# Kernel tuning notes

Hardware: AMD Instinct MI355X
Metric: run time of the kernel (lower is better)

The kernel has to match this reference:

```python
import jax, jax.numpy as jnp
import numpy as np

TEMP_MIN, TEMP_MAX = 0.1, 1.0
NEG = -1e30  # finite stand-in for -inf (grad-safe)


def _cumlse(x, axis, reverse=False):
    # cumulative logsumexp along `axis`
    return jax.lax.associative_scan(jnp.logaddexp, x, axis=axis, reverse=reverse)


def setup_inputs() -> dict:
    key = jax.random.key(0)
    k1, k2, k3 = jax.random.split(key, 3)
    B, T, M, C = 16, 512, 2048, 512
    return {
        "text_embeddings": jax.random.normal(k1, (B, T, C), jnp.float32),
        "mel_embeddings": jax.random.normal(k2, (B, M, C), jnp.float32),
        "noise_uniform": jax.random.uniform(k3, (B, T, M), jnp.float32, 1e-6, 1.0 - 1e-6),
        "temperature_ratio": jnp.full((1,), 0.5, jnp.float32),
    }


def reference(text_embeddings, mel_embeddings, noise_uniform, temperature_ratio):
    B, T, C = text_embeddings.shape
    M, Cm = mel_embeddings.shape[1], mel_embeddings.shape[2]
    energy = jnp.einsum('btc,bmc->btm', text_embeddings, mel_embeddings) / np.float32(np.sqrt(C * Cm))
    temperature = TEMP_MIN + (TEMP_MAX - TEMP_MIN) * jnp.reshape(temperature_ratio, ())
    gumbel = -jnp.log(-jnp.log(noise_uniform))
    # torch code computes e = exp((energy+noise)/T); we keep it in log domain:
    log_e = (energy + gumbel) / temperature                      # [B,T,M]
    # log_cond_prob[b,t,k,j] = log_e[b,t,k] - log_S[b,t,j] if k>=j else -inf
    # (the torch 4D triu-masked tensor, never materialized here)
    log_S = _cumlse(log_e, axis=2, reverse=True)                 # log sum_{k>=j} e[b,t,k]

    # alpha DP: alpha[b,i,k+1] = lse_{j<=k}(alpha[b,i-1,j] + lcp[b,i-1,k,j])
    #         = log_e[b,i-1,k] + lse_{j<=k}(alpha[b,i-1,j] - log_S[b,i-1,j])
    alpha0 = jnp.concatenate([jnp.zeros((B, 1), log_e.dtype),
                              jnp.full((B, M), NEG, log_e.dtype)], axis=1)  # [B,M+1]
    def alpha_step(prev, xs):
        le_t, ls_t = xs                                          # [B,M] each
        inner = _cumlse(prev[:, :M] - ls_t, axis=1)              # lse over j<=k
        new = jnp.concatenate([jnp.full((B, 1), NEG, le_t.dtype), le_t + inner], axis=1)
        return new, new
    _, alphas = jax.lax.scan(alpha_step, alpha0,
                             (jnp.swapaxes(log_e, 0, 1), jnp.swapaxes(log_S, 0, 1)))
    alpha_tail = jnp.swapaxes(alphas, 0, 1)[:, :, 1:]            # alpha[:,1:,1:] -> [B,T,M]

    # beta DP (intended backward recurrence; torch source had an undefined
    # `cond_prob` and a shape bug here):
    # beta[b,i,j] = lse_{k>=j}(beta[b,i+1,k] + log_e[b,i,k]) - log_S[b,i,j]
    beta_T = jnp.zeros((B, M), log_e.dtype).at[:, M - 1].set(1.0)  # faithful odd init =1
    def beta_step(nxt, xs):
        le_t, ls_t = xs
        new = _cumlse(nxt + le_t, axis=1, reverse=True) - ls_t
        return new, new
    _, betas = jax.lax.scan(beta_step, beta_T,
                            (jnp.swapaxes(log_e, 0, 1)[:T - 1], jnp.swapaxes(log_S, 0, 1)[:T - 1]),
                            reverse=True)
    beta = jnp.swapaxes(jnp.concatenate([betas, beta_T[None]], axis=0), 0, 1)  # [B,T,M]

    gamma = alpha_tail + beta
    gamma_log = gamma - jax.scipy.special.logsumexp(gamma, axis=1, keepdims=True)
    # torch uses raw (log-domain) gamma in the bmm; kept faithful
    expanded = jnp.einsum('btm,btc->bmc', gamma, text_embeddings)  # [B,M,C]
    return gamma_log, expanded
```

## Files before the change

### kernel.cpp

```cpp
#include <hip/hip_runtime.h>

#define B_  16
#define T_  512
#define M_  2048
#define C_  512
#define NEGV (-1e30f)
#define L2E 1.4426950408889634f
#define LN2 0.69314718055994531f

typedef unsigned short u16;
typedef unsigned int   u32;
using bf16x8 = __attribute__((ext_vector_type(8))) short;
using f32x4  = __attribute__((ext_vector_type(4))) float;

__device__ __forceinline__ u16 f2bf(float x) {
  u32 u = __float_as_uint(x);
  return (u16)((u + 0x7FFFu + ((u >> 16) & 1u)) >> 16);
}
__device__ __forceinline__ float bf2f(u16 u) {
  return __uint_as_float(((u32)u) << 16);
}
__device__ __forceinline__ float rdlane63(float x) {
  return __int_as_float(__builtin_amdgcn_readlane(__float_as_int(x), 63));
}

__device__ __forceinline__ float wscan_add(float x) {
  x += __int_as_float(__builtin_amdgcn_update_dpp(0, __float_as_int(x), 0x111, 0xF, 0xF, true));
  x += __int_as_float(__builtin_amdgcn_update_dpp(0, __float_as_int(x), 0x112, 0xF, 0xF, true));
  x += __int_as_float(__builtin_amdgcn_update_dpp(0, __float_as_int(x), 0x114, 0xF, 0xF, true));
  x += __int_as_float(__builtin_amdgcn_update_dpp(0, __float_as_int(x), 0x118, 0xF, 0xF, true));
  x += __int_as_float(__builtin_amdgcn_update_dpp(0, __float_as_int(x), 0x142, 0xA, 0xF, true));
  x += __int_as_float(__builtin_amdgcn_update_dpp(0, __float_as_int(x), 0x143, 0xC, 0xF, true));
  return x;
}
__device__ __forceinline__ float dpp_shr1(float x) {
  return __int_as_float(__builtin_amdgcn_update_dpp(0, __float_as_int(x), 0x138, 0xF, 0xF, true));
}

__launch_bounds__(256)
__global__ void k1_energy(const float* __restrict__ text, const float* __restrict__ mel,
                          const float* __restrict__ noise, const float* __restrict__ ratio,
                          u16* __restrict__ ttbuf)
{
  __shared__ __align__(16) short As[128][40];
  __shared__ __align__(16) short Bs[128][40];
  const int b   = blockIdx.z;
  const int t0  = blockIdx.x * 128;
  const int m0  = blockIdx.y * 128;
  const int tid = threadIdx.x;
  const int lane = tid & 63, wid = tid >> 6;
  const int wr = wid >> 1, wc = wid & 1;
  const float* Ab = text + (size_t)b * T_ * C_;
  const float* Bb = mel  + (size_t)b * M_ * C_;
  f32x4 acc[4][4];
#pragma unroll
  for (int i = 0; i < 4; ++i)
#pragma unroll
    for (int j = 0; j < 4; ++j) acc[i][j] = (f32x4){0.f, 0.f, 0.f, 0.f};

  const int kq = (tid & 7) * 4;
  const int rb = tid >> 3;
  for (int kk = 0; kk < C_; kk += 32) {
    __syncthreads();
#pragma unroll
    for (int it = 0; it < 4; ++it) {
      int r = rb + it * 32;
      float4 va = *(const float4*)(Ab + (size_t)(t0 + r) * C_ + kk + kq);
      As[r][kq + 0] = (short)f2bf(va.x); As[r][kq + 1] = (short)f2bf(va.y);
      As[r][kq + 2] = (short)f2bf(va.z); As[r][kq + 3] = (short)f2bf(va.w);
      float4 vb = *(const float4*)(Bb + (size_t)(m0 + r) * C_ + kk + kq);
      Bs[r][kq + 0] = (short)f2bf(vb.x); Bs[r][kq + 1] = (short)f2bf(vb.y);
      Bs[r][kq + 2] = (short)f2bf(vb.z); Bs[r][kq + 3] = (short)f2bf(vb.w);
    }
    __syncthreads();
    const int k0 = (lane >> 4) * 8;
    bf16x8 af[4], bfr[4];
#pragma unroll
    for (int i = 0; i < 4; ++i) {
      af[i]  = *(const bf16x8*)&As[wr * 64 + i * 16 + (lane & 15)][k0];
      bfr[i] = *(const bf16x8*)&Bs[wc * 64 + i * 16 + (lane & 15)][k0];
    }
#pragma unroll
    for (int i = 0; i < 4; ++i)
#pragma unroll
      for (int j = 0; j < 4; ++j)
        acc[i][j] = __builtin_amdgcn_mfma_f32_16x16x32_bf16(af[i], bfr[j], acc[i][j], 0, 0, 0);
  }
  const float invT = 1.0f / (0.1f + 0.9f * ratio[0]);
  const float D2 = 14.5f * invT * L2E;
#pragma unroll
  for (int i = 0; i < 4; ++i) {
#pragma unroll
    for (int j = 0; j < 4; ++j) {
#pragma unroll
      for (int rr = 0; rr < 4; ++rr) {
        int t = t0 + wr * 64 + i * 16 + (lane >> 4) * 4 + rr;
        int m = m0 + wc * 64 + j * 16 + (lane & 15);
        size_t idx = ((size_t)b * T_ + t) * M_ + m;
        float en = acc[i][j][rr] * (1.0f / 512.0f);
        float u  = noise[idx];
        float nl = -LN2 * __builtin_amdgcn_logf(u);
        float g  = -LN2 * __builtin_amdgcn_logf(nl);
        float le = (en + g) * invT;
        float tv = __builtin_amdgcn_exp2f(__builtin_fmaf(le, L2E, -D2));
        ttbuf[idx] = f2bf(tv);
      }
    }
  }
}

__launch_bounds__(256)
__global__ void k2r(const u16* __restrict__ ttbuf, u16* __restrict__ Rbuf)
{
  const size_t row = blockIdx.x;
  const u16* src = ttbuf + row * M_;
  u16* dst = Rbuf + row * M_;
  const int tid = threadIdx.x, lane = tid & 63, wid = tid >> 6;
  const int c0 = tid * 8;
  uint4 w = *(const uint4*)(src + c0);
  float x[8];
  x[0] = __uint_as_float(w.x << 16); x[1] = __uint_as_float(w.x & 0xFFFF0000u);
  x[2] = __uint_as_float(w.y << 16); x[3] = __uint_as_float(w.y & 0xFFFF0000u);
  x[4] = __uint_as_float(w.z << 16); x[5] = __uint_as_float(w.z & 0xFFFF0000u);
  x[6] = __uint_as_float(w.w << 16); x[7] = __uint_as_float(w.w & 0xFFFF0000u);
#pragma unroll
  for (int i = 6; i >= 0; --i) x[i] += x[i + 1];
  float v = x[0];
#pragma unroll
  for (int d = 1; d < 64; d <<= 1) {
    float t = __shfl_down(v, d);
    if (lane < 64 - d) v += t;
  }
  float e = __shfl_down(v, 1);
  if (lane == 63) e = 0.f;
  __shared__ float part[4];
  if (lane == 0) part[wid] = v;
  __syncthreads();
  float we = 0.f;
  for (int w2 = wid + 1; w2 < 4; ++w2) we += part[w2];
  float off = e + we;
  u32 o[4];
#pragma unroll
  for (int i = 0; i < 4; ++i) {
    float r0 = __builtin_amdgcn_rcpf(x[2*i]     + off);
    float r1 = __builtin_amdgcn_rcpf(x[2*i + 1] + off);
    o[i] = __builtin_amdgcn_perm(__float_as_uint(r1), __float_as_uint(r0), 0x07060302u);
  }
  *(uint4*)(dst + c0) = make_uint4(o[0], o[1], o[2], o[3]);
}

__launch_bounds__(512)
__global__ void k3a_partial(const float* __restrict__ text, float* __restrict__ partial)
{
  const int b = blockIdx.x >> 3, ch = blockIdx.x & 7, c = threadIdx.x;
  const float* tb = text + (size_t)b * T_ * C_ + (size_t)ch * 64 * C_ + c;
  float s = 0.f;
#pragma unroll 8
  for (int tt = 0; tt < 64; ++tt) s += tb[(size_t)tt * C_];
  partial[((size_t)b * 8 + ch) * C_ + c] = s;
}

__launch_bounds__(512)
__global__ void k3b_suffix(const float* __restrict__ text, const float* __restrict__ partial,
                           float* __restrict__ suffix)
{
  const int b = blockIdx.x >> 3, ch = blockIdx.x & 7, c = threadIdx.x;
  float off = 0.f;
  for (int ch2 = ch + 1; ch2 < 8; ++ch2) off += partial[((size_t)b * 8 + ch2) * C_ + c];
  const float* tb = text + (size_t)b * T_ * C_ + (size_t)ch * 64 * C_ + c;
  float* sb = suffix + (size_t)b * (T_ + 1) * C_ + (size_t)ch * 64 * C_ + c;
  if (ch == 7) sb[(size_t)64 * C_] = 0.f;
  float s = off;
  for (int tt = 63; tt >= 0; --tt) {
    s += tb[(size_t)tt * C_];
    sb[(size_t)tt * C_] = s;
  }
}

__launch_bounds__(256)
__global__ void k3t_textT(const float* __restrict__ text, u16* __restrict__ textT)
{
  __shared__ u16 tile[64][66];
  const int b  = blockIdx.z;
  const int t0 = blockIdx.x * 64;
  const int c0 = blockIdx.y * 64;
  const int tid = threadIdx.x;
  const int j = tid & 63, i4 = tid >> 6;
#pragma unroll
  for (int it = 0; it < 16; ++it) {
    int i = it * 4 + i4;
    tile[i][j] = f2bf(text[((size_t)b * T_ + t0 + i) * C_ + c0 + j]);
  }
  __syncthreads();
#pragma unroll
  for (int it = 0; it < 16; ++it) {
    int cc = it * 4 + i4;
    textT[((size_t)b * C_ + c0 + cc) * T_ + t0 + j] = tile[j][cc];
  }
}

__launch_bounds__(64, 1)
__global__ void k4_dp(const u16* __restrict__ ttbuf, const u16* __restrict__ Rbuf,
                      u16* __restrict__ Abuf, u16* __restrict__ Bbuf,
                      float* __restrict__ CAa, float* __restrict__ CBa)
{
  const int blk = blockIdx.x;
  const int b   = blk & 15;
  const int lane = threadIdx.x & 63;
  const u16* TT = ttbuf + (size_t)b * T_ * M_;
  const u16* RR = Rbuf  + (size_t)b * T_ * M_;
  uint4 rawT[2][4], rawR[2][4];
  float arr[32], cum[32], A[32];
  float Cv = 0.f;

  if (blk < 16) {
    const int c0 = lane * 32;
    u16* AO = Abuf + (size_t)b * T_ * M_;
    float* CO = CAa + (size_t)b * T_;

#define TLDA(BUF, R) { \
    const uint4* pt_ = (const uint4*)(TT + (size_t)(R) * M_ + c0); \
    const uint4* pr_ = (const uint4*)(RR + (size_t)(R) * M_ + c0); \
    rawT[BUF][0]=pt_[0]; rawT[BUF][1]=pt_[1]; rawT[BUF][2]=pt_[2]; rawT[BUF][3]=pt_[3]; \
    rawR[BUF][0]=pr_[0]; rawR[BUF][1]=pr_[1]; rawR[BUF][2]=pr_[2]; rawR[BUF][3]=pr_[3]; }

#define FOLD2A(E, W) { \
    cum[E]   = A[(E)-1] * __uint_as_float((W) << 16); \
    cum[(E)+1] = A[E]   * __uint_as_float((W) & 0xFFFF0000u); }

#define ASTEP(BUF, RIDX, FIRST) { \
    const int r_ = (RIDX); \
     \
    _Pragma("unroll") for (int q = 0; q < 4; ++q) { \
      u32 w0 = rawT[BUF][q].x, w1 = rawT[BUF][q].y, w2 = rawT[BUF][q].z, w3 = rawT[BUF][q].w; \
      arr[8*q+0] = __uint_as_float(w0 << 16); arr[8*q+1] = __uint_as_float(w0 & 0xFFFF0000u); \
      arr[8*q+2] = __uint_as_float(w1 << 16); arr[8*q+3] = __uint_as_float(w1 & 0xFFFF0000u); \
      arr[8*q+4] = __uint_as_float(w2 << 16); arr[8*q+5] = __uint_as_float(w2 & 0xFFFF0000u); \
      arr[8*q+6] = __uint_as_float(w3 << 16); arr[8*q+7] = __uint_as_float(w3 & 0xFFFF0000u); } \
     \
    { float am1 = dpp_shr1(A[31]); \
      if (FIRST) am1 = (lane == 0) ? 1.f : am1; \
      u32 v0 = rawR[BUF][0].x; \
      cum[0] = am1 * __uint_as_float(v0 << 16); \
      cum[1] = A[0] * __uint_as_float(v0 & 0xFFFF0000u); } \
    FOLD2A(2, rawR[BUF][0].y) FOLD2A(4, rawR[BUF][0].z) FOLD2A(6, rawR[BUF][0].w) \
    _Pragma("unroll") for (int q = 1; q < 4; ++q) { \
      FOLD2A(8*q+0, rawR[BUF][q].x) FOLD2A(8*q+2, rawR[BUF][q].y) \
      FOLD2A(8*q+4, rawR[BUF][q].z) FOLD2A(8*q+6, rawR[BUF][q].w) } \
     \
    TLDA(BUF, (r_ + 2 < T_) ? r_ + 2 : T_ - 1) \
    __builtin_amdgcn_sched_barrier(0); \
     \
    _Pragma("unroll") for (int c = 0; c < 4; ++c) \
      _Pragma("unroll") for (int k = 1; k < 8; ++k) cum[8*c+k] += cum[8*c+k-1]; \
    { float Te = (cum[7] + cum[15]) + (cum[23] + cum[31]); \
      float v_ = wscan_add(Te); \
      float exw = v_ - Te; \
      float Zt = rdlane63(v_); \
      float f0 = exw, f1 = f0+cum[7], f2 = f1+cum[15], f3 = f2+cum[23]; \
      float Zc = fmaxf(Zt, 1e-35f); \
      float zr = __builtin_amdgcn_rcpf(Zc); \
      Cv += LN2 * __builtin_amdgcn_logf(Zc); \
      if (lane == 0) CO[r_] = Cv; \
      float fz0 = f0*zr, fz1 = f1*zr, fz2 = f2*zr, fz3 = f3*zr; \
      _Pragma("unroll") for (int k = 0; k < 8; ++k) { \
        A[k]    = arr[k]    * __builtin_fmaf(cum[k],    zr, fz0); \
        A[8+k]  = arr[8+k]  * __builtin_fmaf(cum[8+k],  zr, fz1); \
        A[16+k] = arr[16+k] * __builtin_fmaf(cum[16+k], zr, fz2); \
        A[24+k] = arr[24+k] * __builtin_fmaf(cum[24+k], zr, fz3); } } \
    { u32 w_[16]; \
      _Pragma("unroll") for (int d = 0; d < 16; ++d) \
        w_[d] = __builtin_amdgcn_perm(__float_as_uint(A[2*d+1]), __float_as_uint(A[2*d]), 0x07060302u); \
      uint4* op = (uint4*)(AO + (size_t)r_ * M_ + c0); \
      op[0] = make_uint4(w_[0],w_[1],w_[2],w_[3]); \
      op[1] = make_uint4(w_[4],w_[5],w_[6],w_[7]); \
      op[2] = make_uint4(w_[8],w_[9],w_[10],w_[11]); \
      op[3] = make_uint4(w_[12],w_[13],w_[14],w_[15]); } \
  }

#pragma unroll
    for (int e = 0; e < 32; ++e) A[e] = 0.f;
    TLDA(0, 0) TLDA(1, 1)
    ASTEP(0, 0, true)
    ASTEP(1, 1, false)
    for (int r = 2; r < T_; r += 2) {
      ASTEP(0, r, false)
      ASTEP(1, r + 1, false)
    }
  } else {
    const int jb = M_ - 32 - lane * 32;
    u16* BO = Bbuf + (size_t)b * T_ * M_;
    float* CO = CBa + (size_t)b * T_;

#define TLDB(BUF, R) { \
    const uint4* pt_ = (const uint4*)(TT + (size_t)(R) * M_ + jb); \
    const uint4* pr_ = (const uint4*)(RR + (size_t)(R) * M_ + jb); \
    rawT[BUF][0]=pt_[0]; rawT[BUF][1]=pt_[1]; rawT[BUF][2]=pt_[2]; rawT[BUF][3]=pt_[3]; \
    rawR[BUF][0]=pr_[0]; rawR[BUF][1]=pr_[1]; rawR[BUF][2]=pr_[2]; rawR[BUF][3]=pr_[3]; }

#define FOLD2B(E, W) { \
    cum[E]     = A[E]     * __uint_as_float((W) << 16); \
    cum[(E)-1] = A[(E)-1] * __uint_as_float((W) & 0xFFFF0000u); }

#define BSTEP(BUF, TIDX) { \
    const int t_ = (TIDX); \
     \
    _Pragma("unroll") for (int q = 0; q < 4; ++q) { \
      u32 w0 = rawR[BUF][q].x, w1 = rawR[BUF][q].y, w2 = rawR[BUF][q].z, w3 = rawR[BUF][q].w; \
      arr[31-8*q] = __uint_as_float(w0 << 16); arr[30-8*q] = __uint_as_float(w0 & 0xFFFF0000u); \
      arr[29-8*q] = __uint_as_float(w1 << 16); arr[28-8*q] = __uint_as_float(w1 & 0xFFFF0000u); \
      arr[27-8*q] = __uint_as_float(w2 << 16); arr[26-8*q] = __uint_as_float(w2 & 0xFFFF0000u); \
      arr[25-8*q] = __uint_as_float(w3 << 16); arr[24-8*q] = __uint_as_float(w3 & 0xFFFF0000u); } \
     \
    _Pragma("unroll") for (int q = 0; q < 4; ++q) { \
      FOLD2B(31-8*q, rawT[BUF][q].x) FOLD2B(29-8*q, rawT[BUF][q].y) \
      FOLD2B(27-8*q, rawT[BUF][q].z) FOLD2B(25-8*q, rawT[BUF][q].w) } \
    { int tp_ = t_ - 2; if (tp_ < 0) tp_ = 0; TLDB(BUF, tp_) } \
    __builtin_amdgcn_sched_barrier(0); \
     \
    _Pragma("unroll") for (int c = 0; c < 4; ++c) \
      _Pragma("unroll") for (int k = 1; k < 8; ++k) cum[8*c+k] += cum[8*c+k-1]; \
    { float Te = (cum[7] + cum[15]) + (cum[23] + cum[31]); \
      float v_ = wscan_add(Te); \
      float exw = v_ - Te; \
      float Zb = rdlane63(v_); \
      float f0 = exw, f1 = f0+cum[7], f2 = f1+cum[15], f3 = f2+cum[23]; \
      float Zc = fmaxf(Zb, 1e-35f); \
      float zr = __builtin_amdgcn_rcpf(Zc); \
      Cv += LN2 * __builtin_amdgcn_logf(Zc); \
      float fz0 = f0*zr, fz1 = f1*zr, fz2 = f2*zr, fz3 = f3*zr; \
      _Pragma("unroll") for (int k = 0; k < 8; ++k) { \
        A[k]    = arr[k]    * __builtin_fmaf(cum[k],    zr, fz0); \
        A[8+k]  = arr[8+k]  * __builtin_fmaf(cum[8+k],  zr, fz1); \
        A[16+k] = arr[16+k] * __builtin_fmaf(cum[16+k], zr, fz2); \
        A[24+k] = arr[24+k] * __builtin_fmaf(cum[24+k], zr, fz3); } } \
    if (t_ >= 0) { \
      if (lane == 0) CO[t_] = Cv; \
      u32 w_[16]; \
      _Pragma("unroll") for (int d = 0; d < 16; ++d) \
        w_[d] = __builtin_amdgcn_perm(__float_as_uint(A[30-2*d]), __float_as_uint(A[31-2*d]), 0x07060302u); \
      uint4* op = (uint4*)(BO + (size_t)t_ * M_ + jb); \
      op[0] = make_uint4(w_[0],w_[1],w_[2],w_[3]); \
      op[1] = make_uint4(w_[4],w_[5],w_[6],w_[7]); \
      op[2] = make_uint4(w_[8],w_[9],w_[10],w_[11]); \
      op[3] = make_uint4(w_[12],w_[13],w_[14],w_[15]); } \
  }

#pragma unroll
    for (int e = 0; e < 32; ++e) A[e] = 1.f;
    if (lane == 0) A[0] = 2.718281828f;
    { u32 w_[16];
#pragma unroll
      for (int d = 0; d < 16; ++d)
        w_[d] = __builtin_amdgcn_perm(__float_as_uint(A[30-2*d]), __float_as_uint(A[31-2*d]), 0x07060302u);
      uint4* op = (uint4*)(BO + (size_t)(T_ - 1) * M_ + jb);
      op[0] = make_uint4(w_[0],w_[1],w_[2],w_[3]);
      op[1] = make_uint4(w_[4],w_[5],w_[6],w_[7]);
      op[2] = make_uint4(w_[8],w_[9],w_[10],w_[11]);
      op[3] = make_uint4(w_[12],w_[13],w_[14],w_[15]);
      if (lane == 0) CO[T_ - 1] = 0.f;
    }
    TLDB(0, T_ - 2) TLDB(1, T_ - 3)
    BSTEP(0, T_ - 2)
    BSTEP(1, T_ - 3)
    for (int t = T_ - 4; t >= 0; t -= 2) {
      BSTEP(0, t)
      BSTEP(1, t - 1)
    }
  }
}

__launch_bounds__(256)
__global__ void k6_combine(const u16* __restrict__ Abuf, const u16* __restrict__ Bbuf,
                           const float* __restrict__ CAa, const float* __restrict__ CBa,
                           float* __restrict__ gamma_log, u16* __restrict__ gammaT)
{
  __shared__ u16 gst[32][514];
  __shared__ float cd[T_];
  __shared__ float smx[8][32], ssm[8][32];
  const int b  = blockIdx.x >> 6;
  const int m0 = (blockIdx.x & 63) * 32;
  const int tid = threadIdx.x;
  const int mi = tid & 31, ti = tid >> 5;
  const int m = m0 + mi;
  const size_t base = (size_t)b * T_ * M_ + m;

  cd[tid]       = CAa[b * T_ + tid]       + CBa[b * T_ + tid];
  cd[tid + 256] = CAa[b * T_ + tid + 256] + CBa[b * T_ + tid + 256];
  __syncthreads();

  float mx = -3.0e38f, s = 0.f;
  for (int t = ti; t < T_; t += 8) {
    float a  = bf2f(Abuf[base + (size_t)t * M_]);
    float bb = bf2f(Bbuf[base + (size_t)t * M_]);
    float g;
    if (t <= m) {
      g = __builtin_fmaf(__builtin_amdgcn_logf(a) + __builtin_amdgcn_logf(bb), LN2, cd[t]);
      g = fmaxf(g, -1e8f);
    } else g = NEGV;
    gst[mi][t] = f2bf(g);
    if (g > mx) { s = s * __builtin_amdgcn_exp2f((mx - g) * L2E) + 1.f; mx = g; }
    else        { s += __builtin_amdgcn_exp2f((g - mx) * L2E); }
  }
  smx[ti][mi] = mx; ssm[ti][mi] = s;
  __syncthreads();
  float Mv = smx[0][mi], Sv = ssm[0][mi];
#pragma unroll
  for (int k = 1; k < 8; ++k) {
    float Mk = smx[k][mi], Sk = ssm[k][mi];
    if (Mk > Mv) { Sv = Sv * __builtin_amdgcn_exp2f((Mv - Mk) * L2E) + Sk; Mv = Mk; }
    else         { Sv += Sk * __builtin_amdgcn_exp2f((Mk - Mv) * L2E); }
  }
  const float lse = Mv + LN2 * __builtin_amdgcn_logf(Sv);

  for (int t = ti; t < T_; t += 8) {
    float g = (t <= m) ? bf2f(gst[mi][t]) : NEGV;
    gamma_log[base + (size_t)t * M_] = g - lse;
  }
  for (int k = 0; k < 32; ++k) {
    u32 val = *(const u32*)&gst[k][2 * tid];
    int mr = m0 + k;
    u32 lo = (2 * tid     <= mr) ? (val & 0x0000FFFFu) : 0u;
    u32 hi = (2 * tid + 1 <= mr) ? (val & 0xFFFF0000u) : 0u;
    ((u32*)gammaT)[((((size_t)b * M_ + m0 + k) * T_) >> 1) + tid] = lo | hi;
  }
}

__launch_bounds__(256)
__global__ void k7_expanded(const u16* __restrict__ gammaT, const u16* __restrict__ textT,
                            const float* __restrict__ suffix, float* __restrict__ expanded)
{
  __shared__ __align__(16) short As[128][40];
  __shared__ __align__(16) short Bs[128][40];
  const int b   = blockIdx.z;
  const int m0  = blockIdx.x * 128;
  const int c0  = blockIdx.y * 128;
  const int tid = threadIdx.x;
  const int lane = tid & 63, wid = tid >> 6;
  const int wr = wid >> 1, wc = wid & 1;
  const u16* Ab = gammaT + (size_t)b * M_ * T_;
  const u16* Bb = textT  + (size_t)b * C_ * T_;
  f32x4 acc[4][4];
#pragma unroll
  for (int i = 0; i < 4; ++i)
#pragma unroll
    for (int j = 0; j < 4; ++j) acc[i][j] = (f32x4){0.f, 0.f, 0.f, 0.f};

  const int ko  = (tid & 3) * 8;
  const int rb2 = tid >> 2;
  for (int kk = 0; kk < T_; kk += 32) {
    __syncthreads();
#pragma unroll
    for (int it = 0; it < 2; ++it) {
      int r = rb2 + it * 64;
      *(uint4*)&As[r][ko] = *(const uint4*)(Ab + (size_t)(m0 + r) * T_ + kk + ko);
      *(uint4*)&Bs[r][ko] = *(const uint4*)(Bb + (size_t)(c0 + r) * T_ + kk + ko);
    }
    __syncthreads();
    const int k0 = (lane >> 4) * 8;
    bf16x8 af[4], bfr[4];
#pragma unroll
    for (int i = 0; i < 4; ++i) {
      af[i]  = *(const bf16x8*)&As[wr * 64 + i * 16 + (lane & 15)][k0];
      bfr[i] = *(const bf16x8*)&Bs[wc * 64 + i * 16 + (lane & 15)][k0];
    }
#pragma unroll
    for (int i = 0; i < 4; ++i)
#pragma unroll
      for (int j = 0; j < 4; ++j)
        acc[i][j] = __builtin_amdgcn_mfma_f32_16x16x32_bf16(af[i], bfr[j], acc[i][j], 0, 0, 0);
  }
#pragma unroll
  for (int i = 0; i < 4; ++i) {
#pragma unroll
    for (int j = 0; j < 4; ++j) {
#pragma unroll
      for (int rr = 0; rr < 4; ++rr) {
        int m = m0 + wr * 64 + i * 16 + (lane >> 4) * 4 + rr;
        int c = c0 + wc * 64 + j * 16 + (lane & 15);
        int sidx = (m + 1 < T_) ? (m + 1) : T_;
        float sfx = suffix[((size_t)b * (T_ + 1) + sidx) * C_ + c];
        expanded[((size_t)b * M_ + m) * C_ + c] = acc[i][j][rr] + NEGV * sfx;
      }
    }
  }
}

extern "C" void kernel_launch(void* const* d_in, const int* in_sizes, int n_in,
                              void* d_out, int out_size, void* d_ws, size_t ws_size,
                              hipStream_t stream) {
  const float* text  = (const float*)d_in[0];
  const float* mel   = (const float*)d_in[1];
  const float* noise = (const float*)d_in[2];
  const float* ratio = (const float*)d_in[3];

  const size_t BTM = (size_t)B_ * T_ * M_;
  float* out       = (float*)d_out;
  float* gamma_log = out;
  float* expanded  = out + BTM;

  char* w = (char*)d_ws;
  u16*   ttbuf  = (u16*)  (w + 0);
  u16*   Rbuf   = (u16*)  (w + 33554432);
  float* suffix = (float*)(w + 67108864);
  u16*   textT  = (u16*)  (w + 83918848);
  u16*   gammaT = (u16*)  (w + 92307456);
  u16*   Abuf   = (u16*)  (w + 125861888);
  u16*   Bbuf   = (u16*)  (w + 159416320);
  float* partial = (float*)(w + 92307456);
  float* CAa = expanded;
  float* CBa = expanded + (size_t)B_ * T_;

  k3a_partial<<<B_ * 8,          512, 0, stream>>>(text, partial);
  k3b_suffix <<<B_ * 8,          512, 0, stream>>>(text, partial, suffix);
  k3t_textT  <<<dim3(8, 8, 16),  256, 0, stream>>>(text, textT);
  k1_energy  <<<dim3(4, 16, 16), 256, 0, stream>>>(text, mel, noise, ratio, ttbuf);
  k2r        <<<B_ * T_,         256, 0, stream>>>(ttbuf, Rbuf);
  k4_dp      <<<32,               64, 0, stream>>>(ttbuf, Rbuf, Abuf, Bbuf, CAa, CBa);
  k6_combine <<<B_ * 64,         256, 0, stream>>>(Abuf, Bbuf, CAa, CBa, gamma_log, gammaT);
  k7_expanded<<<dim3(16, 4, 16), 256, 0, stream>>>(gammaT, textT, suffix, expanded);
}
```

Before: 457.5 us.

## Store DP intermediates in fp32 and triple-buffer the alpha/beta prefetch

Energy exponentials and reciprocal suffix sums are now stored as fp32 instead of bf16, which removes the unpacking work in the DP kernel. The alpha and beta recurrences prefetch three rows ahead with three register buffers, and the beta pass uses natural ordering inside each lane. Workspace is repacked so Bbuf and the normaliser arrays live in the output buffer. This doubles bytes moved for these intermediates and raises register pressure in the serial DP.

```diff
diff --git a/kernel.cpp b/kernel.cpp
--- a/kernel.cpp
+++ b/kernel.cpp
@@ -40,7 +40,7 @@
 __launch_bounds__(256)
 __global__ void k1_energy(const float* __restrict__ text, const float* __restrict__ mel,
                           const float* __restrict__ noise, const float* __restrict__ ratio,
-                          u16* __restrict__ ttbuf)
+                          float* __restrict__ ttbuf)
 {
   __shared__ __align__(16) short As[128][40];
   __shared__ __align__(16) short Bs[128][40];
@@ -102,27 +102,25 @@
         float nl = -LN2 * __builtin_amdgcn_logf(u);
         float g  = -LN2 * __builtin_amdgcn_logf(nl);
         float le = (en + g) * invT;
-        float tv = __builtin_amdgcn_exp2f(__builtin_fmaf(le, L2E, -D2));
-        ttbuf[idx] = f2bf(tv);
+        ttbuf[idx] = __builtin_amdgcn_exp2f(__builtin_fmaf(le, L2E, -D2));
       }
     }
   }
 }
 
 __launch_bounds__(256)
-__global__ void k2r(const u16* __restrict__ ttbuf, u16* __restrict__ Rbuf)
+__global__ void k2r(const float* __restrict__ ttbuf, float* __restrict__ Rbuf)
 {
   const size_t row = blockIdx.x;
-  const u16* src = ttbuf + row * M_;
-  u16* dst = Rbuf + row * M_;
+  const float* src = ttbuf + row * M_;
+  float* dst = Rbuf + row * M_;
   const int tid = threadIdx.x, lane = tid & 63, wid = tid >> 6;
   const int c0 = tid * 8;
-  uint4 w = *(const uint4*)(src + c0);
   float x[8];
-  x[0] = __uint_as_float(w.x << 16); x[1] = __uint_as_float(w.x & 0xFFFF0000u);
-  x[2] = __uint_as_float(w.y << 16); x[3] = __uint_as_float(w.y & 0xFFFF0000u);
-  x[4] = __uint_as_float(w.z << 16); x[5] = __uint_as_float(w.z & 0xFFFF0000u);
-  x[6] = __uint_as_float(w.w << 16); x[7] = __uint_as_float(w.w & 0xFFFF0000u);
+  float4 xa = *(const float4*)(src + c0);
+  float4 xb = *(const float4*)(src + c0 + 4);
+  x[0] = xa.x; x[1] = xa.y; x[2] = xa.z; x[3] = xa.w;
+  x[4] = xb.x; x[5] = xb.y; x[6] = xb.z; x[7] = xb.w;
 #pragma unroll
   for (int i = 6; i >= 0; --i) x[i] += x[i + 1];
   float v = x[0];
@@ -139,14 +137,17 @@
   float we = 0.f;
   for (int w2 = wid + 1; w2 < 4; ++w2) we += part[w2];
   float off = e + we;
-  u32 o[4];
-#pragma unroll
-  for (int i = 0; i < 4; ++i) {
-    float r0 = __builtin_amdgcn_rcpf(x[2*i]     + off);
-    float r1 = __builtin_amdgcn_rcpf(x[2*i + 1] + off);
-    o[i] = __builtin_amdgcn_perm(__float_as_uint(r1), __float_as_uint(r0), 0x07060302u);
-  }
-  *(uint4*)(dst + c0) = make_uint4(o[0], o[1], o[2], o[3]);
+  float4 r0, r1;
+  r0.x = __builtin_amdgcn_rcpf(x[0] + off);
+  r0.y = __builtin_amdgcn_rcpf(x[1] + off);
+  r0.z = __builtin_amdgcn_rcpf(x[2] + off);
+  r0.w = __builtin_amdgcn_rcpf(x[3] + off);
+  r1.x = __builtin_amdgcn_rcpf(x[4] + off);
+  r1.y = __builtin_amdgcn_rcpf(x[5] + off);
+  r1.z = __builtin_amdgcn_rcpf(x[6] + off);
+  r1.w = __builtin_amdgcn_rcpf(x[7] + off);
+  *(float4*)(dst + c0)     = r0;
+  *(float4*)(dst + c0 + 4) = r1;
 }
 
 __launch_bounds__(512)
@@ -200,17 +201,16 @@
 }
 
 __launch_bounds__(64, 1)
-__global__ void k4_dp(const u16* __restrict__ ttbuf, const u16* __restrict__ Rbuf,
+__global__ void k4_dp(const float* __restrict__ ttbuf, const float* __restrict__ Rbuf,
                       u16* __restrict__ Abuf, u16* __restrict__ Bbuf,
                       float* __restrict__ CAa, float* __restrict__ CBa)
 {
   const int blk = blockIdx.x;
   const int b   = blk & 15;
   const int lane = threadIdx.x & 63;
-  const u16* TT = ttbuf + (size_t)b * T_ * M_;
-  const u16* RR = Rbuf  + (size_t)b * T_ * M_;
-  uint4 rawT[2][4], rawR[2][4];
-  float arr[32], cum[32], A[32];
+  const float* TTf = ttbuf + (size_t)b * T_ * M_;
+  const float* RRf = Rbuf  + (size_t)b * T_ * M_;
+  float ttb[3][32], Rb[3][32], cum[32], A[32];
   float Cv = 0.f;
 
   if (blk < 16) {
@@ -219,55 +219,35 @@
     float* CO = CAa + (size_t)b * T_;
 
 #define TLDA(BUF, R) { \
-    const uint4* pt_ = (const uint4*)(TT + (size_t)(R) * M_ + c0); \
-    const uint4* pr_ = (const uint4*)(RR + (size_t)(R) * M_ + c0); \
-    rawT[BUF][0]=pt_[0]; rawT[BUF][1]=pt_[1]; rawT[BUF][2]=pt_[2]; rawT[BUF][3]=pt_[3]; \
-    rawR[BUF][0]=pr_[0]; rawR[BUF][1]=pr_[1]; rawR[BUF][2]=pr_[2]; rawR[BUF][3]=pr_[3]; }
-
-#define FOLD2A(E, W) { \
-    cum[E]   = A[(E)-1] * __uint_as_float((W) << 16); \
-    cum[(E)+1] = A[E]   * __uint_as_float((W) & 0xFFFF0000u); }
+    const float4* pt_ = (const float4*)(TTf + (size_t)(R) * M_ + c0); \
+    const float4* pr_ = (const float4*)(RRf + (size_t)(R) * M_ + c0); \
+    _Pragma("unroll") for (int g = 0; g < 8; ++g) { \
+      *(float4*)&ttb[BUF][4*g] = pt_[g]; \
+      *(float4*)&Rb[BUF][4*g]  = pr_[g]; } }
 
 #define ASTEP(BUF, RIDX, FIRST) { \
     const int r_ = (RIDX); \
-     \
-    _Pragma("unroll") for (int q = 0; q < 4; ++q) { \
-      u32 w0 = rawT[BUF][q].x, w1 = rawT[BUF][q].y, w2 = rawT[BUF][q].z, w3 = rawT[BUF][q].w; \
-      arr[8*q+0] = __uint_as_float(w0 << 16); arr[8*q+1] = __uint_as_float(w0 & 0xFFFF0000u); \
-      arr[8*q+2] = __uint_as_float(w1 << 16); arr[8*q+3] = __uint_as_float(w1 & 0xFFFF0000u); \
-      arr[8*q+4] = __uint_as_float(w2 << 16); arr[8*q+5] = __uint_as_float(w2 & 0xFFFF0000u); \
-      arr[8*q+6] = __uint_as_float(w3 << 16); arr[8*q+7] = __uint_as_float(w3 & 0xFFFF0000u); } \
-     \
-    { float am1 = dpp_shr1(A[31]); \
-      if (FIRST) am1 = (lane == 0) ? 1.f : am1; \
-      u32 v0 = rawR[BUF][0].x; \
-      cum[0] = am1 * __uint_as_float(v0 << 16); \
-      cum[1] = A[0] * __uint_as_float(v0 & 0xFFFF0000u); } \
-    FOLD2A(2, rawR[BUF][0].y) FOLD2A(4, rawR[BUF][0].z) FOLD2A(6, rawR[BUF][0].w) \
-    _Pragma("unroll") for (int q = 1; q < 4; ++q) { \
-      FOLD2A(8*q+0, rawR[BUF][q].x) FOLD2A(8*q+2, rawR[BUF][q].y) \
-      FOLD2A(8*q+4, rawR[BUF][q].z) FOLD2A(8*q+6, rawR[BUF][q].w) } \
-     \
-    TLDA(BUF, (r_ + 2 < T_) ? r_ + 2 : T_ - 1) \
-    __builtin_amdgcn_sched_barrier(0); \
-     \
+    float am1 = dpp_shr1(A[31]); \
+    if (FIRST) am1 = (lane == 0) ? 1.f : am1; \
+    cum[0] = am1 * Rb[BUF][0]; \
+    _Pragma("unroll") for (int e = 1; e < 32; ++e) cum[e] = A[e-1] * Rb[BUF][e]; \
     _Pragma("unroll") for (int c = 0; c < 4; ++c) \
       _Pragma("unroll") for (int k = 1; k < 8; ++k) cum[8*c+k] += cum[8*c+k-1]; \
-    { float Te = (cum[7] + cum[15]) + (cum[23] + cum[31]); \
-      float v_ = wscan_add(Te); \
-      float exw = v_ - Te; \
-      float Zt = rdlane63(v_); \
-      float f0 = exw, f1 = f0+cum[7], f2 = f1+cum[15], f3 = f2+cum[23]; \
-      float Zc = fmaxf(Zt, 1e-35f); \
-      float zr = __builtin_amdgcn_rcpf(Zc); \
-      Cv += LN2 * __builtin_amdgcn_logf(Zc); \
-      if (lane == 0) CO[r_] = Cv; \
-      float fz0 = f0*zr, fz1 = f1*zr, fz2 = f2*zr, fz3 = f3*zr; \
-      _Pragma("unroll") for (int k = 0; k < 8; ++k) { \
-        A[k]    = arr[k]    * __builtin_fmaf(cum[k],    zr, fz0); \
-        A[8+k]  = arr[8+k]  * __builtin_fmaf(cum[8+k],  zr, fz1); \
-        A[16+k] = arr[16+k] * __builtin_fmaf(cum[16+k], zr, fz2); \
-        A[24+k] = arr[24+k] * __builtin_fmaf(cum[24+k], zr, fz3); } } \
+    float lt = (cum[7] + cum[15]) + (cum[23] + cum[31]); \
+    float v_ = wscan_add(lt); \
+    float exw = v_ - lt; \
+    float Zt = rdlane63(v_); \
+    float f0 = exw, f1 = f0 + cum[7], f2 = f1 + cum[15], f3 = f2 + cum[23]; \
+    float Zc = fmaxf(Zt, 1e-35f); \
+    float zr = __builtin_amdgcn_rcpf(Zc); \
+    Cv += LN2 * __builtin_amdgcn_logf(Zc); \
+    if (lane == 0) CO[r_] = Cv; \
+    float fz0 = f0*zr, fz1 = f1*zr, fz2 = f2*zr, fz3 = f3*zr; \
+    _Pragma("unroll") for (int k = 0; k < 8; ++k) { \
+      A[k]    = ttb[BUF][k]    * __builtin_fmaf(cum[k],    zr, fz0); \
+      A[8+k]  = ttb[BUF][8+k]  * __builtin_fmaf(cum[8+k],  zr, fz1); \
+      A[16+k] = ttb[BUF][16+k] * __builtin_fmaf(cum[16+k], zr, fz2); \
+      A[24+k] = ttb[BUF][24+k] * __builtin_fmaf(cum[24+k], zr, fz3); } \
     { u32 w_[16]; \
       _Pragma("unroll") for (int d = 0; d < 16; ++d) \
         w_[d] = __builtin_amdgcn_perm(__float_as_uint(A[2*d+1]), __float_as_uint(A[2*d]), 0x07060302u); \
@@ -276,83 +256,74 @@
       op[1] = make_uint4(w_[4],w_[5],w_[6],w_[7]); \
       op[2] = make_uint4(w_[8],w_[9],w_[10],w_[11]); \
       op[3] = make_uint4(w_[12],w_[13],w_[14],w_[15]); } \
+    TLDA(BUF, (r_ + 3 < T_) ? r_ + 3 : T_ - 1) \
+    __builtin_amdgcn_sched_barrier(0); \
   }
 
 #pragma unroll
     for (int e = 0; e < 32; ++e) A[e] = 0.f;
-    TLDA(0, 0) TLDA(1, 1)
+    TLDA(0, 0) TLDA(1, 1) TLDA(2, 2)
     ASTEP(0, 0, true)
     ASTEP(1, 1, false)
-    for (int r = 2; r < T_; r += 2) {
-      ASTEP(0, r, false)
+    ASTEP(2, 2, false)
+    for (int r = 3; r + 2 < T_; r += 3) {
+      ASTEP(0, r,     false)
       ASTEP(1, r + 1, false)
-    }
+      ASTEP(2, r + 2, false)
+    }
+    ASTEP(0, T_ - 2, false)
+    ASTEP(1, T_ - 1, false)
   } else {
     const int jb = M_ - 32 - lane * 32;
     u16* BO = Bbuf + (size_t)b * T_ * M_;
     float* CO = CBa + (size_t)b * T_;
 
 #define TLDB(BUF, R) { \
-    const uint4* pt_ = (const uint4*)(TT + (size_t)(R) * M_ + jb); \
-    const uint4* pr_ = (const uint4*)(RR + (size_t)(R) * M_ + jb); \
-    rawT[BUF][0]=pt_[0]; rawT[BUF][1]=pt_[1]; rawT[BUF][2]=pt_[2]; rawT[BUF][3]=pt_[3]; \
-    rawR[BUF][0]=pr_[0]; rawR[BUF][1]=pr_[1]; rawR[BUF][2]=pr_[2]; rawR[BUF][3]=pr_[3]; }
-
-#define FOLD2B(E, W) { \
-    cum[E]     = A[E]     * __uint_as_float((W) << 16); \
-    cum[(E)-1] = A[(E)-1] * __uint_as_float((W) & 0xFFFF0000u); }
+    const float4* pt_ = (const float4*)(TTf + (size_t)(R) * M_ + jb); \
+    const float4* pr_ = (const float4*)(RRf + (size_t)(R) * M_ + jb); \
+    _Pragma("unroll") for (int g = 0; g < 8; ++g) { \
+      *(float4*)&ttb[BUF][4*g] = pt_[g]; \
+      *(float4*)&Rb[BUF][4*g]  = pr_[g]; } }
 
 #define BSTEP(BUF, TIDX) { \
     const int t_ = (TIDX); \
-     \
-    _Pragma("unroll") for (int q = 0; q < 4; ++q) { \
-      u32 w0 = rawR[BUF][q].x, w1 = rawR[BUF][q].y, w2 = rawR[BUF][q].z, w3 = rawR[BUF][q].w; \
-      arr[31-8*q] = __uint_as_float(w0 << 16); arr[30-8*q] = __uint_as_float(w0 & 0xFFFF0000u); \
-      arr[29-8*q] = __uint_as_float(w1 << 16); arr[28-8*q] = __uint_as_float(w1 & 0xFFFF0000u); \
-      arr[27-8*q] = __uint_as_float(w2 << 16); arr[26-8*q] = __uint_as_float(w2 & 0xFFFF0000u); \
-      arr[25-8*q] = __uint_as_float(w3 << 16); arr[24-8*q] = __uint_as_float(w3 & 0xFFFF0000u); } \
-     \
-    _Pragma("unroll") for (int q = 0; q < 4; ++q) { \
-      FOLD2B(31-8*q, rawT[BUF][q].x) FOLD2B(29-8*q, rawT[BUF][q].y) \
-      FOLD2B(27-8*q, rawT[BUF][q].z) FOLD2B(25-8*q, rawT[BUF][q].w) } \
-    { int tp_ = t_ - 2; if (tp_ < 0) tp_ = 0; TLDB(BUF, tp_) } \
-    __builtin_amdgcn_sched_barrier(0); \
-     \
+    _Pragma("unroll") for (int e = 0; e < 32; ++e) cum[e] = A[e] * ttb[BUF][e]; \
     _Pragma("unroll") for (int c = 0; c < 4; ++c) \
-      _Pragma("unroll") for (int k = 1; k < 8; ++k) cum[8*c+k] += cum[8*c+k-1]; \
-    { float Te = (cum[7] + cum[15]) + (cum[23] + cum[31]); \
-      float v_ = wscan_add(Te); \
-      float exw = v_ - Te; \
-      float Zb = rdlane63(v_); \
-      float f0 = exw, f1 = f0+cum[7], f2 = f1+cum[15], f3 = f2+cum[23]; \
-      float Zc = fmaxf(Zb, 1e-35f); \
-      float zr = __builtin_amdgcn_rcpf(Zc); \
-      Cv += LN2 * __builtin_amdgcn_logf(Zc); \
-      float fz0 = f0*zr, fz1 = f1*zr, fz2 = f2*zr, fz3 = f3*zr; \
-      _Pragma("unroll") for (int k = 0; k < 8; ++k) { \
-        A[k]    = arr[k]    * __builtin_fmaf(cum[k],    zr, fz0); \
-        A[8+k]  = arr[8+k]  * __builtin_fmaf(cum[8+k],  zr, fz1); \
-        A[16+k] = arr[16+k] * __builtin_fmaf(cum[16+k], zr, fz2); \
-        A[24+k] = arr[24+k] * __builtin_fmaf(cum[24+k], zr, fz3); } } \
-    if (t_ >= 0) { \
-      if (lane == 0) CO[t_] = Cv; \
-      u32 w_[16]; \
+      _Pragma("unroll") for (int k = 6; k >= 0; --k) cum[8*c+k] += cum[8*c+k+1]; \
+    float lt = (cum[0] + cum[8]) + (cum[16] + cum[24]); \
+    float v_ = wscan_add(lt); \
+    float exw = v_ - lt; \
+    float Zb = rdlane63(v_); \
+    float f0 = exw, f1 = f0 + cum[24], f2 = f1 + cum[16], f3 = f2 + cum[8]; \
+    float Zc = fmaxf(Zb, 1e-35f); \
+    float zr = __builtin_amdgcn_rcpf(Zc); \
+    Cv += LN2 * __builtin_amdgcn_logf(Zc); \
+    if (lane == 0) CO[t_] = Cv; \
+    float fz0 = f0*zr, fz1 = f1*zr, fz2 = f2*zr, fz3 = f3*zr; \
+    _Pragma("unroll") for (int k = 0; k < 8; ++k) { \
+      A[24+k] = Rb[BUF][24+k] * __builtin_fmaf(cum[24+k], zr, fz0); \
+      A[16+k] = Rb[BUF][16+k] * __builtin_fmaf(cum[16+k], zr, fz1); \
+      A[8+k]  = Rb[BUF][8+k]  * __builtin_fmaf(cum[8+k],  zr, fz2); \
+      A[k]    = Rb[BUF][k]    * __builtin_fmaf(cum[k],    zr, fz3); } \
+    { u32 w_[16]; \
       _Pragma("unroll") for (int d = 0; d < 16; ++d) \
-        w_[d] = __builtin_amdgcn_perm(__float_as_uint(A[30-2*d]), __float_as_uint(A[31-2*d]), 0x07060302u); \
+        w_[d] = __builtin_amdgcn_perm(__float_as_uint(A[2*d+1]), __float_as_uint(A[2*d]), 0x07060302u); \
       uint4* op = (uint4*)(BO + (size_t)t_ * M_ + jb); \
       op[0] = make_uint4(w_[0],w_[1],w_[2],w_[3]); \
       op[1] = make_uint4(w_[4],w_[5],w_[6],w_[7]); \
       op[2] = make_uint4(w_[8],w_[9],w_[10],w_[11]); \
       op[3] = make_uint4(w_[12],w_[13],w_[14],w_[15]); } \
+    TLDB(BUF, (t_ - 3 >= 0) ? t_ - 3 : 0) \
+    __builtin_amdgcn_sched_barrier(0); \
   }
 
 #pragma unroll
     for (int e = 0; e < 32; ++e) A[e] = 1.f;
-    if (lane == 0) A[0] = 2.718281828f;
+    if (lane == 0) A[31] = 2.718281828f;
     { u32 w_[16];
 #pragma unroll
       for (int d = 0; d < 16; ++d)
-        w_[d] = __builtin_amdgcn_perm(__float_as_uint(A[30-2*d]), __float_as_uint(A[31-2*d]), 0x07060302u);
+        w_[d] = __builtin_amdgcn_perm(__float_as_uint(A[2*d+1]), __float_as_uint(A[2*d]), 0x07060302u);
       uint4* op = (uint4*)(BO + (size_t)(T_ - 1) * M_ + jb);
       op[0] = make_uint4(w_[0],w_[1],w_[2],w_[3]);
       op[1] = make_uint4(w_[4],w_[5],w_[6],w_[7]);
@@ -360,13 +331,13 @@
       op[3] = make_uint4(w_[12],w_[13],w_[14],w_[15]);
       if (lane == 0) CO[T_ - 1] = 0.f;
     }
-    TLDB(0, T_ - 2) TLDB(1, T_ - 3)
-    BSTEP(0, T_ - 2)
-    BSTEP(1, T_ - 3)
-    for (int t = T_ - 4; t >= 0; t -= 2) {
+    TLDB(0, T_ - 2) TLDB(1, T_ - 3) TLDB(2, T_ - 4)
+    for (int t = T_ - 2; t >= 2; t -= 3) {
       BSTEP(0, t)
       BSTEP(1, t - 1)
-    }
+      BSTEP(2, t - 2)
+    }
+    BSTEP(0, 0)
   }
 }
 
@@ -500,16 +471,16 @@
   float* expanded  = out + BTM;
 
   char* w = (char*)d_ws;
-  u16*   ttbuf  = (u16*)  (w + 0);
-  u16*   Rbuf   = (u16*)  (w + 33554432);
-  float* suffix = (float*)(w + 67108864);
-  u16*   textT  = (u16*)  (w + 83918848);
-  u16*   gammaT = (u16*)  (w + 92307456);
-  u16*   Abuf   = (u16*)  (w + 125861888);
-  u16*   Bbuf   = (u16*)  (w + 159416320);
-  float* partial = (float*)(w + 92307456);
-  float* CAa = expanded;
-  float* CBa = expanded + (size_t)B_ * T_;
+  float* ttbuf  = (float*)(w + 0);
+  float* Rbuf   = (float*)(w + 67108864);
+  float* suffix = (float*)(w + 134217728);
+  u16*   textT  = (u16*)  (w + 151027712);
+  u16*   Abuf   = (u16*)  (w + 159416320);
+  u16*   gammaT = (u16*)  (w + 0);
+  float* partial = (float*)(w + 67108864);
+  u16*   Bbuf = (u16*)expanded;
+  float* CAa  = (float*)((char*)expanded + 33554432);
+  float* CBa  = CAa + (size_t)B_ * T_;
 
   k3a_partial<<<B_ * 8,          512, 0, stream>>>(text, partial);
   k3b_suffix <<<B_ * 8,          512, 0, stream>>>(text, partial, suffix);
```

New measurement: 628.2 us. 37.3% more time.
